# Kernel optimization log

Hardware: AMD Instinct MI355X
Metric: run time of the kernel (lower is better)

Reference implementation:

```python
import jax, jax.numpy as jnp
import numpy as np

BS, T_SEG, C, D, N, K, H = 4, 16, 64, 64, 4096, 32, 64
STRIDE = 4
NB, BSZ, NG, BPG = 4, 8, 1, 4  # K = NB*BSZ, NB = NG*BPG (dendritic tree covers all K)
EPS = 1e-8


def _forward(cc_signals, h_prev, prev_messages, trace_prim, trace_key,
             primitives, key_p, decay_logit, dendrite_branch_w, dendrite_group_w,
             fc1_w, fc1_b, fc2_w, fc2_b, mod_lr_logit, conn_indices):
    bs, n, d = h_prev.shape
    # ---- per-neuron modulator MLP: [h, trace_prim, trace_key, primitives, key] -> 3 ----
    mod_input = jnp.concatenate([
        h_prev, trace_prim, trace_key,
        jnp.broadcast_to(primitives[None], (bs, n, d)),
        jnp.broadcast_to(key_p[None], (bs, n, d))], axis=-1)           # [BS,N,5D]
    x = jnp.tanh(jnp.einsum('bnd,ndh->bnh', mod_input, fc1_w) + fc1_b)  # [BS,N,H]
    out3 = jnp.einsum('bnh,nho->bno', x, fc2_w) + fc2_b                 # [BS,N,3]
    gate_prim = jnp.tanh(out3[..., 0:1])
    gate_key = jnp.tanh(out3[..., 1:2])
    decay_mod = out3[..., 2]

    mod_lr = jax.nn.sigmoid(mod_lr_logit)
    tp_dir = trace_prim / jnp.clip(jnp.linalg.norm(trace_prim, axis=-1, keepdims=True), EPS)
    tk_dir = trace_key / jnp.clip(jnp.linalg.norm(trace_key, axis=-1, keepdims=True), EPS)
    eff_prim = primitives[None] + mod_lr * gate_prim * tp_dir           # [BS,N,D]
    eff_key = key_p[None] + mod_lr * gate_key * tk_dir                  # [BS,N,D]
    eff_decay = jax.nn.sigmoid(decay_logit[None] + decay_mod)[..., None]  # [BS,N,1]

    # routing computed once per segment from the initial messages
    routing = jax.nn.sigmoid(
        jnp.einsum('bnd,bnkd->bnk', eff_key, prev_messages[:, conn_indices]))  # [BS,N,K]

    def gather_fc(weighted):  # [BS,N,K,D] -> [BS,N,D] hierarchical dendritic reduce
        tree = weighted.reshape(bs, n, NB, BSZ, d)
        branch = jnp.tanh(jnp.einsum('bnjkd,njkd->bnjd', tree, dendrite_branch_w))  # [BS,N,NB,D]
        grouped = branch.reshape(bs, n, NG, BPG, d)
        group = jnp.tanh(jnp.einsum('bngpd,ngpd->bngd', grouped, dendrite_group_w))  # [BS,N,NG,D]
        return group.mean(axis=2)  # n_tree == K so no leftover term

    cc_steps = jnp.moveaxis(cc_signals[:, ::STRIDE], 0, 1)  # [n_steps,BS,C,D]

    def step(carry, cc_t):
        h, prev_msg = carry
        nm = prev_msg[:, conn_indices]                      # neighbor gather [BS,N,K,D]
        received = gather_fc(routing[..., None] * nm)       # [BS,N,D]
        received = received.at[:, :C].add(cc_t)             # inject port signals
        h = eff_decay * h + (1.0 - eff_decay) * received
        prev_msg = jnp.tanh(h * eff_prim)
        return (h, prev_msg), prev_msg[:, :C]

    (h_final, _), ports = jax.lax.scan(step, (h_prev, prev_messages), cc_steps)
    # each port output is held for `stride` tokens; only the fresh one carries grad
    ports_rep = jnp.repeat(ports, STRIDE, axis=0)            # [T,BS,C,D]
    fresh = (jnp.arange(T_SEG) % STRIDE == 0)[:, None, None, None]
    out = jnp.where(fresh, ports_rep, jax.lax.stop_gradient(ports_rep))
    return jnp.moveaxis(out, 0, 1)                           # [BS,T_seg,C,D]


def setup_inputs() -> dict:
    key = jax.random.key(0)
    ks = jax.random.split(key, 10)

    def rms_init(k, shape):
        raw = jax.random.normal(k, shape, dtype=jnp.float32)
        rms = jnp.clip(jnp.sqrt(jnp.mean(raw ** 2, axis=-1, keepdims=True)), EPS)
        return raw / rms

    cc_signals = jax.random.normal(ks[0], (BS, T_SEG, C, D), dtype=jnp.float32)
    h_prev = 0.1 * jax.random.normal(ks[1], (BS, N, D), dtype=jnp.float32)
    primitives = rms_init(ks[2], (N, D))
    key_p = rms_init(ks[3], (N, D))
    prev_messages = jnp.tanh(h_prev * primitives[None])
    trace_prim = 0.1 * jax.random.normal(ks[4], (BS, N, D), dtype=jnp.float32)
    trace_key = 0.1 * jax.random.normal(ks[5], (BS, N, D), dtype=jnp.float32)
    decay_logit = jnp.zeros((N,), dtype=jnp.float32)
    dendrite_branch_w = jnp.full((N, NB, BSZ, D), 1.0 / BSZ, dtype=jnp.float32)
    dendrite_group_w = jnp.full((N, NG, BPG, D), 1.0 / BPG, dtype=jnp.float32)
    fc1_w = jax.random.normal(ks[6], (N, 5 * D, H), dtype=jnp.float32) * (2.0 / (5 * D + H)) ** 0.5
    fc1_b = jnp.zeros((N, H), dtype=jnp.float32)
    fc2_w = 0.02 * jax.random.normal(ks[7], (N, H, 3), dtype=jnp.float32)
    fc2_b = jnp.zeros((N, 3), dtype=jnp.float32)
    mod_lr_logit = jnp.float32(-2.0)
    conn_indices = jnp.sort(jax.random.randint(ks[8], (N, K), 0, N, dtype=jnp.int32), axis=-1)
    return dict(cc_signals=cc_signals, h_prev=h_prev, prev_messages=prev_messages,
                trace_prim=trace_prim, trace_key=trace_key, primitives=primitives,
                key_p=key_p, decay_logit=decay_logit,
                dendrite_branch_w=dendrite_branch_w, dendrite_group_w=dendrite_group_w,
                fc1_w=fc1_w, fc1_b=fc1_b, fc2_w=fc2_w, fc2_b=fc2_b,
                mod_lr_logit=mod_lr_logit, conn_indices=conn_indices)


def reference(cc_signals, h_prev, prev_messages, trace_prim, trace_key,
              primitives, key_p, decay_logit, dendrite_branch_w, dendrite_group_w,
              fc1_w, fc1_b, fc2_w, fc2_b, mod_lr_logit, conn_indices):
    return _forward(cc_signals, h_prev, prev_messages, trace_prim, trace_key,
                    primitives, key_p, decay_logit, dendrite_branch_w, dendrite_group_w,
                    fc1_w, fc1_b, fc2_w, fc2_b, mod_lr_logit, conn_indices)
```

## Files before the change

### kernel.cpp

```cpp
#include <hip/hip_runtime.h>
#include <math.h>

#define BS 4
#define TSEG 16
#define CC 64
#define DD 64
#define NN 4096
#define KK 32
#define HH 64
#define D5 320

__device__ __forceinline__ float sigm(float x){ return 1.0f/(1.0f+expf(-x)); }
__device__ __forceinline__ float4 tanh4(float4 v){
    return make_float4(tanhf(v.x), tanhf(v.y), tanhf(v.z), tanhf(v.w));
}

__global__ __launch_bounds__(256) void k_pre(
    const float* __restrict__ h_prev,
    const float* __restrict__ pm0,
    const float* __restrict__ trp,
    const float* __restrict__ trk,
    const float* __restrict__ prim,
    const float* __restrict__ keyp,
    const float* __restrict__ dlog,
    const float* __restrict__ fc1w,
    const float* __restrict__ fc1b,
    const float* __restrict__ fc2w,
    const float* __restrict__ fc2b,
    const float* __restrict__ mll,
    const int*  __restrict__ conn,
    float* __restrict__ ws_ep,
    float* __restrict__ ws_rt,
    float* __restrict__ ws_ed)
{
    __shared__ float mod2[4][D5][4];
    __shared__ float ek_s[4][4][DD];
    __shared__ int   cn_s[4][KK];
    const int wid  = threadIdx.x >> 6;
    const int lane = threadIdx.x & 63;
    const int n    = (blockIdx.x << 2) + wid;

    #pragma unroll
    for (int b = 0; b < BS; b++) {
        mod2[wid][lane      ][b] = h_prev[((size_t)b*NN + n)*DD + lane];
        mod2[wid][64  + lane][b] = trp  [((size_t)b*NN + n)*DD + lane];
        mod2[wid][128 + lane][b] = trk  [((size_t)b*NN + n)*DD + lane];
    }
    {
        const float pv = prim[(size_t)n*DD + lane];
        const float kv = keyp[(size_t)n*DD + lane];
        #pragma unroll
        for (int b = 0; b < BS; b++) {
            mod2[wid][192 + lane][b] = pv;
            mod2[wid][256 + lane][b] = kv;
        }
    }
    if (lane < KK) cn_s[wid][lane] = conn[(size_t)n*KK + lane];

    const int g  = lane >> 4;
    const int hq = lane & 15;
    float acc[16];
    #pragma unroll
    for (int i = 0; i < 16; i++) acc[i] = 0.f;
    const float* wp = fc1w + (size_t)n*D5*HH + (size_t)g*HH + 4*hq;
    const float* mp = &mod2[wid][g][0];
    #pragma unroll 4
    for (int it = 0; it < 80; it++) {
        const float4 w4 = *(const float4*)(wp + (size_t)it*256);
        const float4 m4 = *(const float4*)(mp + it*16);
        acc[ 0] = fmaf(m4.x, w4.x, acc[ 0]);
        acc[ 1] = fmaf(m4.x, w4.y, acc[ 1]);
        acc[ 2] = fmaf(m4.x, w4.z, acc[ 2]);
        acc[ 3] = fmaf(m4.x, w4.w, acc[ 3]);
        acc[ 4] = fmaf(m4.y, w4.x, acc[ 4]);
        acc[ 5] = fmaf(m4.y, w4.y, acc[ 5]);
        acc[ 6] = fmaf(m4.y, w4.z, acc[ 6]);
        acc[ 7] = fmaf(m4.y, w4.w, acc[ 7]);
        acc[ 8] = fmaf(m4.z, w4.x, acc[ 8]);
        acc[ 9] = fmaf(m4.z, w4.y, acc[ 9]);
        acc[10] = fmaf(m4.z, w4.z, acc[10]);
        acc[11] = fmaf(m4.z, w4.w, acc[11]);
        acc[12] = fmaf(m4.w, w4.x, acc[12]);
        acc[13] = fmaf(m4.w, w4.y, acc[13]);
        acc[14] = fmaf(m4.w, w4.z, acc[14]);
        acc[15] = fmaf(m4.w, w4.w, acc[15]);
    }
    #pragma unroll
    for (int i = 0; i < 16; i++) {
        acc[i] += __shfl_xor(acc[i], 16, 64);
        acc[i] += __shfl_xor(acc[i], 32, 64);
    }
    const float4 b1 = *(const float4*)(fc1b + (size_t)n*HH + 4*hq);
    float x[16];
    #pragma unroll
    for (int b = 0; b < BS; b++) {
        x[b*4+0] = tanhf(acc[b*4+0] + b1.x);
        x[b*4+1] = tanhf(acc[b*4+1] + b1.y);
        x[b*4+2] = tanhf(acc[b*4+2] + b1.z);
        x[b*4+3] = tanhf(acc[b*4+3] + b1.w);
    }

    float f2[12];
    {
        const float4* f2p = (const float4*)(fc2w + (size_t)n*HH*3 + 12*hq);
        const float4 fa = f2p[0], fb = f2p[1], fc = f2p[2];
        f2[0]=fa.x; f2[1]=fa.y; f2[2]=fa.z; f2[3]=fa.w;
        f2[4]=fb.x; f2[5]=fb.y; f2[6]=fb.z; f2[7]=fb.w;
        f2[8]=fc.x; f2[9]=fc.y; f2[10]=fc.z; f2[11]=fc.w;
    }
    float po[12];
    #pragma unroll
    for (int b = 0; b < BS; b++) {
        #pragma unroll
        for (int o = 0; o < 3; o++) {
            po[b*3+o] = x[b*4+0]*f2[0*3+o] + x[b*4+1]*f2[1*3+o]
                      + x[b*4+2]*f2[2*3+o] + x[b*4+3]*f2[3*3+o];
        }
    }
    #pragma unroll
    for (int m = 1; m < 16; m <<= 1) {
        #pragma unroll
        for (int i = 0; i < 12; i++) po[i] += __shfl_xor(po[i], m, 64);
    }
    const float c0 = fc2b[(size_t)n*3+0];
    const float c1 = fc2b[(size_t)n*3+1];
    const float c2 = fc2b[(size_t)n*3+2];
    const float dl  = dlog[n];
    const float mlr = sigm(mll[0]);
    float gp[4], gk[4], ed[4];
    #pragma unroll
    for (int b = 0; b < BS; b++) {
        gp[b] = tanhf(po[b*3+0] + c0);
        gk[b] = tanhf(po[b*3+1] + c1);
        ed[b] = sigm(dl + po[b*3+2] + c2);
    }
    if (lane < 4) {
        const float edsel = (lane==0)?ed[0]:(lane==1)?ed[1]:(lane==2)?ed[2]:ed[3];
        ws_ed[(size_t)lane*NN + n] = edsel;
    }

    {
        const int d = lane;
        const float4 tpv = *(const float4*)(&mod2[wid][64  + d][0]);
        const float4 tkv = *(const float4*)(&mod2[wid][128 + d][0]);
        const float  pr  = mod2[wid][192 + d][0];
        const float  kp  = mod2[wid][256 + d][0];
        float tp[4] = {tpv.x, tpv.y, tpv.z, tpv.w};
        float tk[4] = {tkv.x, tkv.y, tkv.z, tkv.w};
        float s2[8];
        #pragma unroll
        for (int b = 0; b < BS; b++) { s2[b] = tp[b]*tp[b]; s2[4+b] = tk[b]*tk[b]; }
        #pragma unroll
        for (int m = 1; m < 64; m <<= 1) {
            #pragma unroll
            for (int i = 0; i < 8; i++) s2[i] += __shfl_xor(s2[i], m, 64);
        }
        #pragma unroll
        for (int b = 0; b < BS; b++) {
            const float np = fmaxf(sqrtf(s2[b]),   1e-8f);
            const float nk = fmaxf(sqrtf(s2[4+b]), 1e-8f);
            const float ep = pr + mlr*gp[b]*(tp[b]/np);
            const float ek = kp + mlr*gk[b]*(tk[b]/nk);
            ws_ep[((size_t)b*NN + n)*DD + d] = ep;
            ek_s[wid][b][d] = ek;
        }
    }

    {
        const int bb = lane >> 4, dq = lane & 15;
        const float4 ekq = *(const float4*)(&ek_s[wid][bb][4*dq]);
        #pragma unroll 8
        for (int k = 0; k < KK; k++) {
            const int cn = cn_s[wid][k];
            const float4 pm4 = *(const float4*)(pm0 + ((size_t)bb*NN + cn)*DD + 4*dq);
            float rr = ekq.x*pm4.x + ekq.y*pm4.y + ekq.z*pm4.z + ekq.w*pm4.w;
            rr += __shfl_xor(rr, 1, 64);
            rr += __shfl_xor(rr, 2, 64);
            rr += __shfl_xor(rr, 4, 64);
            rr += __shfl_xor(rr, 8, 64);
            if (dq == 0) ws_rt[((size_t)bb*NN + n)*KK + k] = sigm(rr);
        }
    }
}

__global__ __launch_bounds__(256) void k_step(
    const float* __restrict__ pm_in,
    float* __restrict__ pm_out,
    const float* __restrict__ h_in,
    float* __restrict__ h_out,
    const float* __restrict__ ws_ep,
    const float* __restrict__ ws_rt,
    const float* __restrict__ ws_ed,
    const float* __restrict__ bw,
    const float* __restrict__ gw,
    const int*  __restrict__ conn,
    const float* __restrict__ cc,
    float* __restrict__ out,
    const int s)
{
    __shared__ float bw_s[4][2048];
    __shared__ float gw_s[4][256];
    __shared__ float rt_s[4][4][KK];
    __shared__ int   cn_s[4][KK];
    const int wid  = threadIdx.x >> 6;
    const int lane = threadIdx.x & 63;
    const int n    = (blockIdx.x << 2) + wid;

    {
        const float4* src = (const float4*)(bw + (size_t)n*2048);
        float4* dst = (float4*)bw_s[wid];
        #pragma unroll
        for (int i = 0; i < 8; i++) dst[i*64 + lane] = src[i*64 + lane];
        ((float4*)gw_s[wid])[lane] = ((const float4*)(gw + (size_t)n*256))[lane];
        rt_s[wid][lane>>5][lane&31] =
            ws_rt[((size_t)(lane>>5)*NN + n)*KK + (lane&31)];
        rt_s[wid][2+(lane>>5)][lane&31] =
            ws_rt[((size_t)(2+(lane>>5))*NN + n)*KK + (lane&31)];
        if (lane < KK) cn_s[wid][lane] = conn[(size_t)n*KK + lane];
    }

    const int b = lane >> 4, dq = lane & 15;
    const int d0 = 4*dq;
    const size_t bnd = ((size_t)b*NN + n)*DD + d0;

    float4 bs[4];
    #pragma unroll
    for (int j = 0; j < 4; j++) bs[j] = make_float4(0.f,0.f,0.f,0.f);
    #pragma unroll
    for (int k = 0; k < KK; k++) {
        const int cn = cn_s[wid][k];
        const float4 nm = *(const float4*)(pm_in + ((size_t)b*NN + cn)*DD + d0);
        const float  w  = rt_s[wid][b][k];
        const float4 bv = *(const float4*)(&bw_s[wid][k*DD + d0]);
        const int j = k >> 3;
        bs[j].x = fmaf(w*nm.x, bv.x, bs[j].x);
        bs[j].y = fmaf(w*nm.y, bv.y, bs[j].y);
        bs[j].z = fmaf(w*nm.z, bv.z, bs[j].z);
        bs[j].w = fmaf(w*nm.w, bv.w, bs[j].w);
    }
    float4 gs = make_float4(0.f,0.f,0.f,0.f);
    #pragma unroll
    for (int j = 0; j < 4; j++) {
        const float4 br = tanh4(bs[j]);
        const float4 gv = *(const float4*)(&gw_s[wid][j*DD + d0]);
        gs.x = fmaf(br.x, gv.x, gs.x);
        gs.y = fmaf(br.y, gv.y, gs.y);
        gs.z = fmaf(br.z, gv.z, gs.z);
        gs.w = fmaf(br.w, gv.w, gs.w);
    }
    float4 recv = tanh4(gs);
    if (n < CC) {
        const float4 cv = *(const float4*)(cc + (size_t)((b*TSEG + 4*s)*CC + n)*DD + d0);
        recv.x += cv.x; recv.y += cv.y; recv.z += cv.z; recv.w += cv.w;
    }
    const float edv = ws_ed[(size_t)b*NN + n];
    float4 h = *(const float4*)(h_in + bnd);
    h.x = edv*h.x + (1.f-edv)*recv.x;
    h.y = edv*h.y + (1.f-edv)*recv.y;
    h.z = edv*h.z + (1.f-edv)*recv.z;
    h.w = edv*h.w + (1.f-edv)*recv.w;
    *(float4*)(h_out + bnd) = h;
    const float4 ep = *(const float4*)(ws_ep + bnd);
    const float4 pm = tanh4(make_float4(h.x*ep.x, h.y*ep.y, h.z*ep.z, h.w*ep.w));
    *(float4*)(pm_out + bnd) = pm;
    if (n < CC) {
        #pragma unroll
        for (int r = 0; r < 4; r++)
            *(float4*)(out + (size_t)((b*TSEG + 4*s + r)*CC + n)*DD + d0) = pm;
    }
}

extern "C" void kernel_launch(void* const* d_in, const int* in_sizes, int n_in,
                              void* d_out, int out_size, void* d_ws, size_t ws_size,
                              hipStream_t stream) {
    const float* cc    = (const float*)d_in[0];
    const float* h_prev= (const float*)d_in[1];
    const float* pm0   = (const float*)d_in[2];
    const float* trp   = (const float*)d_in[3];
    const float* trk   = (const float*)d_in[4];
    const float* prim  = (const float*)d_in[5];
    const float* keyp  = (const float*)d_in[6];
    const float* dlog  = (const float*)d_in[7];
    const float* bw    = (const float*)d_in[8];
    const float* gw    = (const float*)d_in[9];
    const float* fc1w  = (const float*)d_in[10];
    const float* fc1b  = (const float*)d_in[11];
    const float* fc2w  = (const float*)d_in[12];
    const float* fc2b  = (const float*)d_in[13];
    const float* mll   = (const float*)d_in[14];
    const int*   conn  = (const int*)d_in[15];
    float* out = (float*)d_out;

    float* ws   = (float*)d_ws;
    const size_t BND = (size_t)BS*NN*DD;
    float* ws_h  = ws;
    float* ws_ep = ws + BND;
    float* msgA  = ws + 2*BND;
    float* msgB  = ws + 3*BND;
    float* ws_rt = ws + 4*BND;
    float* ws_ed = ws + 4*BND + (size_t)BS*NN*KK;

    k_pre<<<NN/4, 256, 0, stream>>>(h_prev, pm0, trp, trk, prim, keyp, dlog,
                                    fc1w, fc1b, fc2w, fc2b, mll, conn,
                                    ws_ep, ws_rt, ws_ed);

    k_step<<<NN/4, 256, 0, stream>>>(pm0,  msgA, h_prev, ws_h, ws_ep, ws_rt, ws_ed,
                                     bw, gw, conn, cc, out, 0);
    k_step<<<NN/4, 256, 0, stream>>>(msgA, msgB, ws_h, ws_h, ws_ep, ws_rt, ws_ed,
                                     bw, gw, conn, cc, out, 1);
    k_step<<<NN/4, 256, 0, stream>>>(msgB, msgA, ws_h, ws_h, ws_ep, ws_rt, ws_ed,
                                     bw, gw, conn, cc, out, 2);
    k_step<<<NN/4, 256, 0, stream>>>(msgA, msgB, ws_h, ws_h, ws_ep, ws_rt, ws_ed,
                                     bw, gw, conn, cc, out, 3);
}
```

Measured before the change: 618.1 us.

## Fuse pre-pass and four step kernels into one cooperative persistent kernel

Merges the modulator/routing pre-pass and the four recurrent step kernels into a single cooperative kernel that uses grid-wide syncs between steps. h, eff_prim, decay and routing stay in registers or LDS instead of round-tripping through workspace, and the dendrite weights are loaded into shared memory once rather than four times. The fc1 weight stream now uses nontemporal loads. The cost is grid.sync overhead and a residency requirement: 1024 blocks with about 38KB of LDS each must all be co-resident. If the cooperative launch fails, the code falls back to the old multi-kernel path.

Result: slower. 1.577 ms (+155.2%).

```diff
diff --git a/kernel.cpp b/kernel.cpp
--- a/kernel.cpp
+++ b/kernel.cpp
@@ -1,5 +1,8 @@
 #include <hip/hip_runtime.h>
+#include <hip/hip_cooperative_groups.h>
 #include <math.h>
+
+namespace cg = cooperative_groups;
 
 #define BS 4
 #define TSEG 16
@@ -10,12 +13,19 @@
 #define HH 64
 #define D5 320
 
+typedef float nat_f4 __attribute__((ext_vector_type(4)));
+
 __device__ __forceinline__ float sigm(float x){ return 1.0f/(1.0f+expf(-x)); }
 __device__ __forceinline__ float4 tanh4(float4 v){
     return make_float4(tanhf(v.x), tanhf(v.y), tanhf(v.z), tanhf(v.w));
 }
-
-__global__ __launch_bounds__(256) void k_pre(
+__device__ __forceinline__ float4 ntload4(const float* p){
+    nat_f4 v = __builtin_nontemporal_load((const nat_f4*)p);
+    return make_float4(v.x, v.y, v.z, v.w);
+}
+
+__global__ __launch_bounds__(256, 4) void k_fused(
+    const float* __restrict__ cc,
     const float* __restrict__ h_prev,
     const float* __restrict__ pm0,
     const float* __restrict__ trp,
@@ -23,36 +33,45 @@
     const float* __restrict__ prim,
     const float* __restrict__ keyp,
     const float* __restrict__ dlog,
+    const float* __restrict__ bw,
+    const float* __restrict__ gw,
     const float* __restrict__ fc1w,
     const float* __restrict__ fc1b,
     const float* __restrict__ fc2w,
     const float* __restrict__ fc2b,
     const float* __restrict__ mll,
     const int*  __restrict__ conn,
-    float* __restrict__ ws_ep,
-    float* __restrict__ ws_rt,
-    float* __restrict__ ws_ed)
+    float* __restrict__ msgA,
+    float* __restrict__ msgB,
+    float* __restrict__ out)
 {
-    __shared__ float mod2[4][D5][4];
-    __shared__ float ek_s[4][4][DD];
+    __shared__ __align__(16) char smem[36864];
+    __shared__ float rt_s[4][4][KK];
     __shared__ int   cn_s[4][KK];
+    float* mod2 = (float*)smem;
+    float* ep_s = (float*)(smem + 20480);
+    float* bw_s = (float*)smem;
+    float* gw_s = (float*)(smem + 32768);
+
     const int wid  = threadIdx.x >> 6;
     const int lane = threadIdx.x & 63;
     const int n    = (blockIdx.x << 2) + wid;
 
-    #pragma unroll
-    for (int b = 0; b < BS; b++) {
-        mod2[wid][lane      ][b] = h_prev[((size_t)b*NN + n)*DD + lane];
-        mod2[wid][64  + lane][b] = trp  [((size_t)b*NN + n)*DD + lane];
-        mod2[wid][128 + lane][b] = trk  [((size_t)b*NN + n)*DD + lane];
+#define MOD2(d,b) mod2[(((wid)*320 + (d))<<2) + (b)]
+
+    #pragma unroll
+    for (int b = 0; b < BS; b++) {
+        MOD2(lane,       b) = h_prev[((size_t)b*NN + n)*DD + lane];
+        MOD2(64  + lane, b) = trp  [((size_t)b*NN + n)*DD + lane];
+        MOD2(128 + lane, b) = trk  [((size_t)b*NN + n)*DD + lane];
     }
     {
         const float pv = prim[(size_t)n*DD + lane];
         const float kv = keyp[(size_t)n*DD + lane];
         #pragma unroll
         for (int b = 0; b < BS; b++) {
-            mod2[wid][192 + lane][b] = pv;
-            mod2[wid][256 + lane][b] = kv;
+            MOD2(192 + lane, b) = pv;
+            MOD2(256 + lane, b) = kv;
         }
     }
     if (lane < KK) cn_s[wid][lane] = conn[(size_t)n*KK + lane];
@@ -63,10 +82,10 @@
     #pragma unroll
     for (int i = 0; i < 16; i++) acc[i] = 0.f;
     const float* wp = fc1w + (size_t)n*D5*HH + (size_t)g*HH + 4*hq;
-    const float* mp = &mod2[wid][g][0];
+    const float* mp = &MOD2(g, 0);
     #pragma unroll 4
     for (int it = 0; it < 80; it++) {
-        const float4 w4 = *(const float4*)(wp + (size_t)it*256);
+        const float4 w4 = ntload4(wp + (size_t)it*256);
         const float4 m4 = *(const float4*)(mp + it*16);
         acc[ 0] = fmaf(m4.x, w4.x, acc[ 0]);
         acc[ 1] = fmaf(m4.x, w4.y, acc[ 1]);
@@ -134,17 +153,14 @@
         gk[b] = tanhf(po[b*3+1] + c1);
         ed[b] = sigm(dl + po[b*3+2] + c2);
     }
-    if (lane < 4) {
-        const float edsel = (lane==0)?ed[0]:(lane==1)?ed[1]:(lane==2)?ed[2]:ed[3];
-        ws_ed[(size_t)lane*NN + n] = edsel;
-    }
-
+
+    float ekreg[4];
     {
         const int d = lane;
-        const float4 tpv = *(const float4*)(&mod2[wid][64  + d][0]);
-        const float4 tkv = *(const float4*)(&mod2[wid][128 + d][0]);
-        const float  pr  = mod2[wid][192 + d][0];
-        const float  kp  = mod2[wid][256 + d][0];
+        const float4 tpv = *(const float4*)(&MOD2(64  + d, 0));
+        const float4 tkv = *(const float4*)(&MOD2(128 + d, 0));
+        const float  pr  = MOD2(192 + d, 0);
+        const float  kp  = MOD2(256 + d, 0);
         float tp[4] = {tpv.x, tpv.y, tpv.z, tpv.w};
         float tk[4] = {tkv.x, tkv.y, tkv.z, tkv.w};
         float s2[8];
@@ -159,13 +175,216 @@
         for (int b = 0; b < BS; b++) {
             const float np = fmaxf(sqrtf(s2[b]),   1e-8f);
             const float nk = fmaxf(sqrtf(s2[4+b]), 1e-8f);
-            const float ep = pr + mlr*gp[b]*(tp[b]/np);
-            const float ek = kp + mlr*gk[b]*(tk[b]/nk);
-            ws_ep[((size_t)b*NN + n)*DD + d] = ep;
-            ek_s[wid][b][d] = ek;
-        }
-    }
-
+            ep_s[((wid*4 + b)<<6) + d] = pr + mlr*gp[b]*(tp[b]/np);
+            ekreg[b] = kp + mlr*gk[b]*(tk[b]/nk);
+        }
+    }
+
+    {
+        const int d = lane;
+        #pragma unroll
+        for (int b = 0; b < BS; b++) MOD2(64 + d, b) = ekreg[b];
+    }
+    {
+        const int bb = lane >> 4, dq = lane & 15;
+        float ekq[4];
+        #pragma unroll
+        for (int i = 0; i < 4; i++) ekq[i] = MOD2(64 + 4*dq + i, bb);
+        #pragma unroll 8
+        for (int k = 0; k < KK; k++) {
+            const int cn = cn_s[wid][k];
+            const float4 pm4 = *(const float4*)(pm0 + ((size_t)bb*NN + cn)*DD + 4*dq);
+            float rr = ekq[0]*pm4.x + ekq[1]*pm4.y + ekq[2]*pm4.z + ekq[3]*pm4.w;
+            rr += __shfl_xor(rr, 1, 64);
+            rr += __shfl_xor(rr, 2, 64);
+            rr += __shfl_xor(rr, 4, 64);
+            rr += __shfl_xor(rr, 8, 64);
+            if (dq == 0) rt_s[wid][bb][k] = sigm(rr);
+        }
+    }
+
+    const int b  = lane >> 4;
+    const int d0 = 4*(lane & 15);
+    const float edv = (b==0)?ed[0]:(b==1)?ed[1]:(b==2)?ed[2]:ed[3];
+    float4 h, ep4;
+    h.x = MOD2(d0+0, b); h.y = MOD2(d0+1, b);
+    h.z = MOD2(d0+2, b); h.w = MOD2(d0+3, b);
+    ep4 = *(const float4*)(&ep_s[((wid*4 + b)<<6) + d0]);
+
+    __syncthreads();
+
+    {
+        const float4* src = (const float4*)(bw + (size_t)n*2048);
+        float4* dst = (float4*)(bw_s + wid*2048);
+        #pragma unroll
+        for (int i = 0; i < 8; i++) dst[i*64 + lane] = src[i*64 + lane];
+        ((float4*)(gw_s + wid*256))[lane] = ((const float4*)(gw + (size_t)n*256))[lane];
+    }
+
+    cg::grid_group grid = cg::this_grid();
+    const size_t bnd = ((size_t)b*NN + n)*DD + d0;
+    const float* pin = pm0;
+    #pragma unroll
+    for (int s = 0; s < 4; s++) {
+        float4 bsa[4];
+        #pragma unroll
+        for (int j = 0; j < 4; j++) bsa[j] = make_float4(0.f,0.f,0.f,0.f);
+        #pragma unroll
+        for (int k = 0; k < KK; k++) {
+            const int cn = cn_s[wid][k];
+            const float4 nm = *(const float4*)(pin + ((size_t)b*NN + cn)*DD + d0);
+            const float  w  = rt_s[wid][b][k];
+            const float4 bv = *(const float4*)(&bw_s[wid*2048 + k*DD + d0]);
+            const int j = k >> 3;
+            bsa[j].x = fmaf(w*nm.x, bv.x, bsa[j].x);
+            bsa[j].y = fmaf(w*nm.y, bv.y, bsa[j].y);
+            bsa[j].z = fmaf(w*nm.z, bv.z, bsa[j].z);
+            bsa[j].w = fmaf(w*nm.w, bv.w, bsa[j].w);
+        }
+        float4 gs = make_float4(0.f,0.f,0.f,0.f);
+        #pragma unroll
+        for (int j = 0; j < 4; j++) {
+            const float4 br = tanh4(bsa[j]);
+            const float4 gv = *(const float4*)(&gw_s[wid*256 + j*DD + d0]);
+            gs.x = fmaf(br.x, gv.x, gs.x);
+            gs.y = fmaf(br.y, gv.y, gs.y);
+            gs.z = fmaf(br.z, gv.z, gs.z);
+            gs.w = fmaf(br.w, gv.w, gs.w);
+        }
+        float4 recv = tanh4(gs);
+        if (n < CC) {
+            const float4 cv = *(const float4*)(cc + (size_t)((b*TSEG + 4*s)*CC + n)*DD + d0);
+            recv.x += cv.x; recv.y += cv.y; recv.z += cv.z; recv.w += cv.w;
+        }
+        h.x = edv*h.x + (1.f-edv)*recv.x;
+        h.y = edv*h.y + (1.f-edv)*recv.y;
+        h.z = edv*h.z + (1.f-edv)*recv.z;
+        h.w = edv*h.w + (1.f-edv)*recv.w;
+        const float4 pm = tanh4(make_float4(h.x*ep4.x, h.y*ep4.y, h.z*ep4.z, h.w*ep4.w));
+        if (s < 3) {
+            float* pout = (s & 1) ? msgB : msgA;
+            *(float4*)(pout + bnd) = pm;
+        }
+        if (n < CC) {
+            #pragma unroll
+            for (int r = 0; r < 4; r++)
+                *(float4*)(out + (size_t)((b*TSEG + 4*s + r)*CC + n)*DD + d0) = pm;
+        }
+        if (s < 3) {
+            __threadfence();
+            grid.sync();
+            pin = (s & 1) ? msgB : msgA;
+        }
+    }
+#undef MOD2
+}
+
+__global__ __launch_bounds__(256) void k_pre(
+    const float* __restrict__ h_prev, const float* __restrict__ pm0,
+    const float* __restrict__ trp, const float* __restrict__ trk,
+    const float* __restrict__ prim, const float* __restrict__ keyp,
+    const float* __restrict__ dlog, const float* __restrict__ fc1w,
+    const float* __restrict__ fc1b, const float* __restrict__ fc2w,
+    const float* __restrict__ fc2b, const float* __restrict__ mll,
+    const int*  __restrict__ conn, float* __restrict__ ws_ep,
+    float* __restrict__ ws_rt, float* __restrict__ ws_ed)
+{
+    __shared__ float mod2[4][D5][4];
+    __shared__ float ek_s[4][4][DD];
+    __shared__ int   cn_s[4][KK];
+    const int wid  = threadIdx.x >> 6;
+    const int lane = threadIdx.x & 63;
+    const int n    = (blockIdx.x << 2) + wid;
+    #pragma unroll
+    for (int b = 0; b < BS; b++) {
+        mod2[wid][lane      ][b] = h_prev[((size_t)b*NN + n)*DD + lane];
+        mod2[wid][64  + lane][b] = trp  [((size_t)b*NN + n)*DD + lane];
+        mod2[wid][128 + lane][b] = trk  [((size_t)b*NN + n)*DD + lane];
+    }
+    {
+        const float pv = prim[(size_t)n*DD + lane];
+        const float kv = keyp[(size_t)n*DD + lane];
+        #pragma unroll
+        for (int b = 0; b < BS; b++) { mod2[wid][192+lane][b]=pv; mod2[wid][256+lane][b]=kv; }
+    }
+    if (lane < KK) cn_s[wid][lane] = conn[(size_t)n*KK + lane];
+    const int g = lane >> 4, hq = lane & 15;
+    float acc[16];
+    #pragma unroll
+    for (int i = 0; i < 16; i++) acc[i] = 0.f;
+    const float* wp = fc1w + (size_t)n*D5*HH + (size_t)g*HH + 4*hq;
+    const float* mp = &mod2[wid][g][0];
+    #pragma unroll 4
+    for (int it = 0; it < 80; it++) {
+        const float4 w4 = *(const float4*)(wp + (size_t)it*256);
+        const float4 m4 = *(const float4*)(mp + it*16);
+        acc[0]=fmaf(m4.x,w4.x,acc[0]);   acc[1]=fmaf(m4.x,w4.y,acc[1]);
+        acc[2]=fmaf(m4.x,w4.z,acc[2]);   acc[3]=fmaf(m4.x,w4.w,acc[3]);
+        acc[4]=fmaf(m4.y,w4.x,acc[4]);   acc[5]=fmaf(m4.y,w4.y,acc[5]);
+        acc[6]=fmaf(m4.y,w4.z,acc[6]);   acc[7]=fmaf(m4.y,w4.w,acc[7]);
+        acc[8]=fmaf(m4.z,w4.x,acc[8]);   acc[9]=fmaf(m4.z,w4.y,acc[9]);
+        acc[10]=fmaf(m4.z,w4.z,acc[10]); acc[11]=fmaf(m4.z,w4.w,acc[11]);
+        acc[12]=fmaf(m4.w,w4.x,acc[12]); acc[13]=fmaf(m4.w,w4.y,acc[13]);
+        acc[14]=fmaf(m4.w,w4.z,acc[14]); acc[15]=fmaf(m4.w,w4.w,acc[15]);
+    }
+    #pragma unroll
+    for (int i = 0; i < 16; i++) { acc[i]+=__shfl_xor(acc[i],16,64); acc[i]+=__shfl_xor(acc[i],32,64); }
+    const float4 b1 = *(const float4*)(fc1b + (size_t)n*HH + 4*hq);
+    float x[16];
+    #pragma unroll
+    for (int b = 0; b < BS; b++) {
+        x[b*4+0]=tanhf(acc[b*4+0]+b1.x); x[b*4+1]=tanhf(acc[b*4+1]+b1.y);
+        x[b*4+2]=tanhf(acc[b*4+2]+b1.z); x[b*4+3]=tanhf(acc[b*4+3]+b1.w);
+    }
+    float f2[12];
+    {
+        const float4* f2p = (const float4*)(fc2w + (size_t)n*HH*3 + 12*hq);
+        const float4 fa=f2p[0], fb=f2p[1], fc=f2p[2];
+        f2[0]=fa.x; f2[1]=fa.y; f2[2]=fa.z; f2[3]=fa.w;
+        f2[4]=fb.x; f2[5]=fb.y; f2[6]=fb.z; f2[7]=fb.w;
+        f2[8]=fc.x; f2[9]=fc.y; f2[10]=fc.z; f2[11]=fc.w;
+    }
+    float po[12];
+    #pragma unroll
+    for (int b = 0; b < BS; b++)
+        #pragma unroll
+        for (int o = 0; o < 3; o++)
+            po[b*3+o] = x[b*4+0]*f2[o] + x[b*4+1]*f2[3+o] + x[b*4+2]*f2[6+o] + x[b*4+3]*f2[9+o];
+    #pragma unroll
+    for (int m = 1; m < 16; m <<= 1)
+        #pragma unroll
+        for (int i = 0; i < 12; i++) po[i] += __shfl_xor(po[i], m, 64);
+    const float c0=fc2b[(size_t)n*3+0], c1=fc2b[(size_t)n*3+1], c2=fc2b[(size_t)n*3+2];
+    const float dl=dlog[n], mlr=sigm(mll[0]);
+    float gp[4], gk[4], ed[4];
+    #pragma unroll
+    for (int b = 0; b < BS; b++) {
+        gp[b]=tanhf(po[b*3+0]+c0); gk[b]=tanhf(po[b*3+1]+c1); ed[b]=sigm(dl+po[b*3+2]+c2);
+    }
+    if (lane < 4) {
+        const float e=(lane==0)?ed[0]:(lane==1)?ed[1]:(lane==2)?ed[2]:ed[3];
+        ws_ed[(size_t)lane*NN + n] = e;
+    }
+    {
+        const int d = lane;
+        const float4 tpv=*(const float4*)(&mod2[wid][64+d][0]);
+        const float4 tkv=*(const float4*)(&mod2[wid][128+d][0]);
+        const float pr=mod2[wid][192+d][0], kp=mod2[wid][256+d][0];
+        float tp[4]={tpv.x,tpv.y,tpv.z,tpv.w}, tk[4]={tkv.x,tkv.y,tkv.z,tkv.w};
+        float s2[8];
+        #pragma unroll
+        for (int b = 0; b < BS; b++) { s2[b]=tp[b]*tp[b]; s2[4+b]=tk[b]*tk[b]; }
+        #pragma unroll
+        for (int m = 1; m < 64; m <<= 1)
+            #pragma unroll
+            for (int i = 0; i < 8; i++) s2[i] += __shfl_xor(s2[i], m, 64);
+        #pragma unroll
+        for (int b = 0; b < BS; b++) {
+            const float np=fmaxf(sqrtf(s2[b]),1e-8f), nk=fmaxf(sqrtf(s2[4+b]),1e-8f);
+            ws_ep[((size_t)b*NN+n)*DD+d] = pr + mlr*gp[b]*(tp[b]/np);
+            ek_s[wid][b][d] = kp + mlr*gk[b]*(tk[b]/nk);
+        }
+    }
     {
         const int bb = lane >> 4, dq = lane & 15;
         const float4 ekq = *(const float4*)(&ek_s[wid][bb][4*dq]);
@@ -174,91 +393,69 @@
             const int cn = cn_s[wid][k];
             const float4 pm4 = *(const float4*)(pm0 + ((size_t)bb*NN + cn)*DD + 4*dq);
             float rr = ekq.x*pm4.x + ekq.y*pm4.y + ekq.z*pm4.z + ekq.w*pm4.w;
-            rr += __shfl_xor(rr, 1, 64);
-            rr += __shfl_xor(rr, 2, 64);
-            rr += __shfl_xor(rr, 4, 64);
-            rr += __shfl_xor(rr, 8, 64);
+            rr+=__shfl_xor(rr,1,64); rr+=__shfl_xor(rr,2,64);
+            rr+=__shfl_xor(rr,4,64); rr+=__shfl_xor(rr,8,64);
             if (dq == 0) ws_rt[((size_t)bb*NN + n)*KK + k] = sigm(rr);
         }
     }
 }
 
 __global__ __launch_bounds__(256) void k_step(
-    const float* __restrict__ pm_in,
-    float* __restrict__ pm_out,
-    const float* __restrict__ h_in,
-    float* __restrict__ h_out,
-    const float* __restrict__ ws_ep,
-    const float* __restrict__ ws_rt,
-    const float* __restrict__ ws_ed,
-    const float* __restrict__ bw,
-    const float* __restrict__ gw,
-    const int*  __restrict__ conn,
-    const float* __restrict__ cc,
-    float* __restrict__ out,
-    const int s)
+    const float* __restrict__ pm_in, float* __restrict__ pm_out,
+    const float* __restrict__ h_in, float* __restrict__ h_out,
+    const float* __restrict__ ws_ep, const float* __restrict__ ws_rt,
+    const float* __restrict__ ws_ed, const float* __restrict__ bw,
+    const float* __restrict__ gw, const int* __restrict__ conn,
+    const float* __restrict__ cc, float* __restrict__ out, const int s)
 {
     __shared__ float bw_s[4][2048];
     __shared__ float gw_s[4][256];
     __shared__ float rt_s[4][4][KK];
     __shared__ int   cn_s[4][KK];
-    const int wid  = threadIdx.x >> 6;
-    const int lane = threadIdx.x & 63;
-    const int n    = (blockIdx.x << 2) + wid;
-
+    const int wid = threadIdx.x >> 6, lane = threadIdx.x & 63;
+    const int n = (blockIdx.x << 2) + wid;
     {
         const float4* src = (const float4*)(bw + (size_t)n*2048);
         float4* dst = (float4*)bw_s[wid];
         #pragma unroll
         for (int i = 0; i < 8; i++) dst[i*64 + lane] = src[i*64 + lane];
         ((float4*)gw_s[wid])[lane] = ((const float4*)(gw + (size_t)n*256))[lane];
-        rt_s[wid][lane>>5][lane&31] =
-            ws_rt[((size_t)(lane>>5)*NN + n)*KK + (lane&31)];
-        rt_s[wid][2+(lane>>5)][lane&31] =
-            ws_rt[((size_t)(2+(lane>>5))*NN + n)*KK + (lane&31)];
+        rt_s[wid][lane>>5][lane&31] = ws_rt[((size_t)(lane>>5)*NN + n)*KK + (lane&31)];
+        rt_s[wid][2+(lane>>5)][lane&31] = ws_rt[((size_t)(2+(lane>>5))*NN + n)*KK + (lane&31)];
         if (lane < KK) cn_s[wid][lane] = conn[(size_t)n*KK + lane];
     }
-
-    const int b = lane >> 4, dq = lane & 15;
-    const int d0 = 4*dq;
+    const int b = lane >> 4, dq = lane & 15, d0 = 4*dq;
     const size_t bnd = ((size_t)b*NN + n)*DD + d0;
-
-    float4 bs[4];
-    #pragma unroll
-    for (int j = 0; j < 4; j++) bs[j] = make_float4(0.f,0.f,0.f,0.f);
+    float4 bsa[4];
+    #pragma unroll
+    for (int j = 0; j < 4; j++) bsa[j] = make_float4(0.f,0.f,0.f,0.f);
     #pragma unroll
     for (int k = 0; k < KK; k++) {
         const int cn = cn_s[wid][k];
         const float4 nm = *(const float4*)(pm_in + ((size_t)b*NN + cn)*DD + d0);
-        const float  w  = rt_s[wid][b][k];
+        const float w = rt_s[wid][b][k];
         const float4 bv = *(const float4*)(&bw_s[wid][k*DD + d0]);
         const int j = k >> 3;
-        bs[j].x = fmaf(w*nm.x, bv.x, bs[j].x);
-        bs[j].y = fmaf(w*nm.y, bv.y, bs[j].y);
-        bs[j].z = fmaf(w*nm.z, bv.z, bs[j].z);
-        bs[j].w = fmaf(w*nm.w, bv.w, bs[j].w);
+        bsa[j].x=fmaf(w*nm.x,bv.x,bsa[j].x); bsa[j].y=fmaf(w*nm.y,bv.y,bsa[j].y);
+        bsa[j].z=fmaf(w*nm.z,bv.z,bsa[j].z); bsa[j].w=fmaf(w*nm.w,bv.w,bsa[j].w);
     }
     float4 gs = make_float4(0.f,0.f,0.f,0.f);
     #pragma unroll
     for (int j = 0; j < 4; j++) {
-        const float4 br = tanh4(bs[j]);
+        const float4 br = tanh4(bsa[j]);
         const float4 gv = *(const float4*)(&gw_s[wid][j*DD + d0]);
-        gs.x = fmaf(br.x, gv.x, gs.x);
-        gs.y = fmaf(br.y, gv.y, gs.y);
-        gs.z = fmaf(br.z, gv.z, gs.z);
-        gs.w = fmaf(br.w, gv.w, gs.w);
+        gs.x=fmaf(br.x,gv.x,gs.x); gs.y=fmaf(br.y,gv.y,gs.y);
+        gs.z=fmaf(br.z,gv.z,gs.z); gs.w=fmaf(br.w,gv.w,gs.w);
     }
     float4 recv = tanh4(gs);
     if (n < CC) {
         const float4 cv = *(const float4*)(cc + (size_t)((b*TSEG + 4*s)*CC + n)*DD + d0);
-        recv.x += cv.x; recv.y += cv.y; recv.z += cv.z; recv.w += cv.w;
+        recv.x+=cv.x; recv.y+=cv.y; recv.z+=cv.z; recv.w+=cv.w;
     }
     const float edv = ws_ed[(size_t)b*NN + n];
     float4 h = *(const float4*)(h_in + bnd);
-    h.x = edv*h.x + (1.f-edv)*recv.x;
-    h.y = edv*h.y + (1.f-edv)*recv.y;
-    h.z = edv*h.z + (1.f-edv)*recv.z;
-    h.w = edv*h.w + (1.f-edv)*recv.w;
+    h.x=edv*h.x+(1.f-edv)*recv.x; h.y=edv*h.y+(1.f-edv)*recv.y;
+    h.z=edv*h.z+(1.f-edv)*recv.z; h.w=edv*h.w+(1.f-edv)*recv.w;
     *(float4*)(h_out + bnd) = h;
     const float4 ep = *(const float4*)(ws_ep + bnd);
     const float4 pm = tanh4(make_float4(h.x*ep.x, h.y*ep.y, h.z*ep.z, h.w*ep.w));
@@ -291,25 +488,35 @@
     const int*   conn  = (const int*)d_in[15];
     float* out = (float*)d_out;
 
-    float* ws   = (float*)d_ws;
+    float* ws = (float*)d_ws;
     const size_t BND = (size_t)BS*NN*DD;
-    float* ws_h  = ws;
-    float* ws_ep = ws + BND;
-    float* msgA  = ws + 2*BND;
-    float* msgB  = ws + 3*BND;
+    float* msgA  = ws;
+    float* msgB  = ws + BND;
+    float* ws_h  = ws + 2*BND;
+    float* ws_ep = ws + 3*BND;
     float* ws_rt = ws + 4*BND;
     float* ws_ed = ws + 4*BND + (size_t)BS*NN*KK;
 
-    k_pre<<<NN/4, 256, 0, stream>>>(h_prev, pm0, trp, trk, prim, keyp, dlog,
-                                    fc1w, fc1b, fc2w, fc2b, mll, conn,
-                                    ws_ep, ws_rt, ws_ed);
-
-    k_step<<<NN/4, 256, 0, stream>>>(pm0,  msgA, h_prev, ws_h, ws_ep, ws_rt, ws_ed,
-                                     bw, gw, conn, cc, out, 0);
-    k_step<<<NN/4, 256, 0, stream>>>(msgA, msgB, ws_h, ws_h, ws_ep, ws_rt, ws_ed,
-                                     bw, gw, conn, cc, out, 1);
-    k_step<<<NN/4, 256, 0, stream>>>(msgB, msgA, ws_h, ws_h, ws_ep, ws_rt, ws_ed,
-                                     bw, gw, conn, cc, out, 2);
-    k_step<<<NN/4, 256, 0, stream>>>(msgA, msgB, ws_h, ws_h, ws_ep, ws_rt, ws_ed,
-                                     bw, gw, conn, cc, out, 3);
+    void* args[] = { (void*)&cc, (void*)&h_prev, (void*)&pm0, (void*)&trp,
+                     (void*)&trk, (void*)&prim, (void*)&keyp, (void*)&dlog,
+                     (void*)&bw, (void*)&gw, (void*)&fc1w, (void*)&fc1b,
+                     (void*)&fc2w, (void*)&fc2b, (void*)&mll, (void*)&conn,
+                     (void*)&msgA, (void*)&msgB, (void*)&out };
+    hipError_t err = hipLaunchCooperativeKernel((void*)k_fused,
+                                                dim3(NN/4), dim3(256),
+                                                args, 0, stream);
+    if (err != hipSuccess) {
+        (void)hipGetLastError();
+        k_pre<<<NN/4, 256, 0, stream>>>(h_prev, pm0, trp, trk, prim, keyp, dlog,
+                                        fc1w, fc1b, fc2w, fc2b, mll, conn,
+                                        ws_ep, ws_rt, ws_ed);
+        k_step<<<NN/4, 256, 0, stream>>>(pm0,  msgA, h_prev, ws_h, ws_ep, ws_rt, ws_ed,
+                                         bw, gw, conn, cc, out, 0);
+        k_step<<<NN/4, 256, 0, stream>>>(msgA, msgB, ws_h, ws_h, ws_ep, ws_rt, ws_ed,
+                                         bw, gw, conn, cc, out, 1);
+        k_step<<<NN/4, 256, 0, stream>>>(msgB, msgA, ws_h, ws_h, ws_ep, ws_rt, ws_ed,
+                                         bw, gw, conn, cc, out, 2);
+        k_step<<<NN/4, 256, 0, stream>>>(msgA, msgB, ws_h, ws_h, ws_ep, ws_rt, ws_ed,
+                                         bw, gw, conn, cc, out, 3);
+    }
 }
```

## Fuse first recurrent step into precompute kernel, drop LDS weight staging

Applied to the files above, without the earlier changes.

The precompute kernel now also runs step 0, reusing h, ep and routing values already held in shared memory and registers. This removes one launch and the global round trip for those intermediates. The step kernel reads dendrite weights straight from global memory instead of staging them in LDS, which lowers LDS use per block and may allow more blocks to be resident. The fc1 weight stream uses nontemporal loads to avoid polluting the cache. The fused kernel uses more registers and shared memory, which could lower its occupancy.

New measurement: 652.0 us. 5.5% more time.

```diff
diff --git a/kernel.cpp b/kernel.cpp
--- a/kernel.cpp
+++ b/kernel.cpp
@@ -10,12 +10,19 @@
 #define HH 64
 #define D5 320
 
+typedef float nat_f4 __attribute__((ext_vector_type(4)));
+
 __device__ __forceinline__ float sigm(float x){ return 1.0f/(1.0f+expf(-x)); }
 __device__ __forceinline__ float4 tanh4(float4 v){
     return make_float4(tanhf(v.x), tanhf(v.y), tanhf(v.z), tanhf(v.w));
 }
-
-__global__ __launch_bounds__(256) void k_pre(
+__device__ __forceinline__ float4 ntload4(const float* p){
+    nat_f4 v = __builtin_nontemporal_load((const nat_f4*)p);
+    return make_float4(v.x, v.y, v.z, v.w);
+}
+
+__global__ __launch_bounds__(256) void k_pre_step0(
+    const float* __restrict__ cc,
     const float* __restrict__ h_prev,
     const float* __restrict__ pm0,
     const float* __restrict__ trp,
@@ -23,18 +30,25 @@
     const float* __restrict__ prim,
     const float* __restrict__ keyp,
     const float* __restrict__ dlog,
+    const float* __restrict__ bw,
+    const float* __restrict__ gw,
     const float* __restrict__ fc1w,
     const float* __restrict__ fc1b,
     const float* __restrict__ fc2w,
     const float* __restrict__ fc2b,
     const float* __restrict__ mll,
     const int*  __restrict__ conn,
+    float* __restrict__ ws_h,
     float* __restrict__ ws_ep,
     float* __restrict__ ws_rt,
-    float* __restrict__ ws_ed)
+    float* __restrict__ ws_ed,
+    float* __restrict__ msgA,
+    float* __restrict__ out)
 {
     __shared__ float mod2[4][D5][4];
     __shared__ float ek_s[4][4][DD];
+    __shared__ float ep_s[4][4][DD];
+    __shared__ float rt_s[4][4][KK];
     __shared__ int   cn_s[4][KK];
     const int wid  = threadIdx.x >> 6;
     const int lane = threadIdx.x & 63;
@@ -66,24 +80,16 @@
     const float* mp = &mod2[wid][g][0];
     #pragma unroll 4
     for (int it = 0; it < 80; it++) {
-        const float4 w4 = *(const float4*)(wp + (size_t)it*256);
+        const float4 w4 = ntload4(wp + (size_t)it*256);
         const float4 m4 = *(const float4*)(mp + it*16);
-        acc[ 0] = fmaf(m4.x, w4.x, acc[ 0]);
-        acc[ 1] = fmaf(m4.x, w4.y, acc[ 1]);
-        acc[ 2] = fmaf(m4.x, w4.z, acc[ 2]);
-        acc[ 3] = fmaf(m4.x, w4.w, acc[ 3]);
-        acc[ 4] = fmaf(m4.y, w4.x, acc[ 4]);
-        acc[ 5] = fmaf(m4.y, w4.y, acc[ 5]);
-        acc[ 6] = fmaf(m4.y, w4.z, acc[ 6]);
-        acc[ 7] = fmaf(m4.y, w4.w, acc[ 7]);
-        acc[ 8] = fmaf(m4.z, w4.x, acc[ 8]);
-        acc[ 9] = fmaf(m4.z, w4.y, acc[ 9]);
-        acc[10] = fmaf(m4.z, w4.z, acc[10]);
-        acc[11] = fmaf(m4.z, w4.w, acc[11]);
-        acc[12] = fmaf(m4.w, w4.x, acc[12]);
-        acc[13] = fmaf(m4.w, w4.y, acc[13]);
-        acc[14] = fmaf(m4.w, w4.z, acc[14]);
-        acc[15] = fmaf(m4.w, w4.w, acc[15]);
+        acc[0]=fmaf(m4.x,w4.x,acc[0]);   acc[1]=fmaf(m4.x,w4.y,acc[1]);
+        acc[2]=fmaf(m4.x,w4.z,acc[2]);   acc[3]=fmaf(m4.x,w4.w,acc[3]);
+        acc[4]=fmaf(m4.y,w4.x,acc[4]);   acc[5]=fmaf(m4.y,w4.y,acc[5]);
+        acc[6]=fmaf(m4.y,w4.z,acc[6]);   acc[7]=fmaf(m4.y,w4.w,acc[7]);
+        acc[8]=fmaf(m4.z,w4.x,acc[8]);   acc[9]=fmaf(m4.z,w4.y,acc[9]);
+        acc[10]=fmaf(m4.z,w4.z,acc[10]); acc[11]=fmaf(m4.z,w4.w,acc[11]);
+        acc[12]=fmaf(m4.w,w4.x,acc[12]); acc[13]=fmaf(m4.w,w4.y,acc[13]);
+        acc[14]=fmaf(m4.w,w4.z,acc[14]); acc[15]=fmaf(m4.w,w4.w,acc[15]);
     }
     #pragma unroll
     for (int i = 0; i < 16; i++) {
@@ -112,10 +118,9 @@
     #pragma unroll
     for (int b = 0; b < BS; b++) {
         #pragma unroll
-        for (int o = 0; o < 3; o++) {
-            po[b*3+o] = x[b*4+0]*f2[0*3+o] + x[b*4+1]*f2[1*3+o]
-                      + x[b*4+2]*f2[2*3+o] + x[b*4+3]*f2[3*3+o];
-        }
+        for (int o = 0; o < 3; o++)
+            po[b*3+o] = x[b*4+0]*f2[o] + x[b*4+1]*f2[3+o]
+                      + x[b*4+2]*f2[6+o] + x[b*4+3]*f2[9+o];
     }
     #pragma unroll
     for (int m = 1; m < 16; m <<= 1) {
@@ -135,8 +140,8 @@
         ed[b] = sigm(dl + po[b*3+2] + c2);
     }
     if (lane < 4) {
-        const float edsel = (lane==0)?ed[0]:(lane==1)?ed[1]:(lane==2)?ed[2]:ed[3];
-        ws_ed[(size_t)lane*NN + n] = edsel;
+        const float e = (lane==0)?ed[0]:(lane==1)?ed[1]:(lane==2)?ed[2]:ed[3];
+        ws_ed[(size_t)lane*NN + n] = e;
     }
 
     {
@@ -160,34 +165,89 @@
             const float np = fmaxf(sqrtf(s2[b]),   1e-8f);
             const float nk = fmaxf(sqrtf(s2[4+b]), 1e-8f);
             const float ep = pr + mlr*gp[b]*(tp[b]/np);
-            const float ek = kp + mlr*gk[b]*(tk[b]/nk);
+            ep_s[wid][b][d] = ep;
             ws_ep[((size_t)b*NN + n)*DD + d] = ep;
-            ek_s[wid][b][d] = ek;
+            ek_s[wid][b][d] = kp + mlr*gk[b]*(tk[b]/nk);
         }
     }
 
-    {
-        const int bb = lane >> 4, dq = lane & 15;
-        const float4 ekq = *(const float4*)(&ek_s[wid][bb][4*dq]);
+    const int b  = lane >> 4;
+    const int dq = lane & 15;
+    const int d0 = 4*dq;
+    {
+        const float4 ekq = *(const float4*)(&ek_s[wid][b][d0]);
         #pragma unroll 8
         for (int k = 0; k < KK; k++) {
             const int cn = cn_s[wid][k];
-            const float4 pm4 = *(const float4*)(pm0 + ((size_t)bb*NN + cn)*DD + 4*dq);
+            const float4 pm4 = *(const float4*)(pm0 + ((size_t)b*NN + cn)*DD + d0);
             float rr = ekq.x*pm4.x + ekq.y*pm4.y + ekq.z*pm4.z + ekq.w*pm4.w;
             rr += __shfl_xor(rr, 1, 64);
             rr += __shfl_xor(rr, 2, 64);
             rr += __shfl_xor(rr, 4, 64);
             rr += __shfl_xor(rr, 8, 64);
-            if (dq == 0) ws_rt[((size_t)bb*NN + n)*KK + k] = sigm(rr);
+            if (dq == 0) {
+                const float rv = sigm(rr);
+                rt_s[wid][b][k] = rv;
+                ws_rt[((size_t)b*NN + n)*KK + k] = rv;
+            }
         }
+    }
+
+    const size_t bnd = ((size_t)b*NN + n)*DD + d0;
+    const float edv = (b==0)?ed[0]:(b==1)?ed[1]:(b==2)?ed[2]:ed[3];
+    float4 h;
+    h.x = mod2[wid][d0+0][b]; h.y = mod2[wid][d0+1][b];
+    h.z = mod2[wid][d0+2][b]; h.w = mod2[wid][d0+3][b];
+    const float4 ep4 = *(const float4*)(&ep_s[wid][b][d0]);
+
+    float4 bsa[4];
+    #pragma unroll
+    for (int j = 0; j < 4; j++) bsa[j] = make_float4(0.f,0.f,0.f,0.f);
+    #pragma unroll
+    for (int k = 0; k < KK; k++) {
+        const int cn = cn_s[wid][k];
+        const float4 nm = *(const float4*)(pm0 + ((size_t)b*NN + cn)*DD + d0);
+        const float  w  = rt_s[wid][b][k];
+        const float4 bv = *(const float4*)(bw + (size_t)n*2048 + k*DD + d0);
+        const int j = k >> 3;
+        bsa[j].x = fmaf(w*nm.x, bv.x, bsa[j].x);
+        bsa[j].y = fmaf(w*nm.y, bv.y, bsa[j].y);
+        bsa[j].z = fmaf(w*nm.z, bv.z, bsa[j].z);
+        bsa[j].w = fmaf(w*nm.w, bv.w, bsa[j].w);
+    }
+    float4 gs = make_float4(0.f,0.f,0.f,0.f);
+    #pragma unroll
+    for (int j = 0; j < 4; j++) {
+        const float4 br = tanh4(bsa[j]);
+        const float4 gv = *(const float4*)(gw + (size_t)n*256 + j*DD + d0);
+        gs.x = fmaf(br.x, gv.x, gs.x);
+        gs.y = fmaf(br.y, gv.y, gs.y);
+        gs.z = fmaf(br.z, gv.z, gs.z);
+        gs.w = fmaf(br.w, gv.w, gs.w);
+    }
+    float4 recv = tanh4(gs);
+    if (n < CC) {
+        const float4 cv = *(const float4*)(cc + (size_t)((b*TSEG)*CC + n)*DD + d0);
+        recv.x += cv.x; recv.y += cv.y; recv.z += cv.z; recv.w += cv.w;
+    }
+    h.x = edv*h.x + (1.f-edv)*recv.x;
+    h.y = edv*h.y + (1.f-edv)*recv.y;
+    h.z = edv*h.z + (1.f-edv)*recv.z;
+    h.w = edv*h.w + (1.f-edv)*recv.w;
+    *(float4*)(ws_h + bnd) = h;
+    const float4 pm = tanh4(make_float4(h.x*ep4.x, h.y*ep4.y, h.z*ep4.z, h.w*ep4.w));
+    *(float4*)(msgA + bnd) = pm;
+    if (n < CC) {
+        #pragma unroll
+        for (int r = 0; r < 4; r++)
+            *(float4*)(out + (size_t)((b*TSEG + r)*CC + n)*DD + d0) = pm;
     }
 }
 
 __global__ __launch_bounds__(256) void k_step(
     const float* __restrict__ pm_in,
     float* __restrict__ pm_out,
-    const float* __restrict__ h_in,
-    float* __restrict__ h_out,
+    float* __restrict__ ws_h,
     const float* __restrict__ ws_ep,
     const float* __restrict__ ws_rt,
     const float* __restrict__ ws_ed,
@@ -198,51 +258,41 @@
     float* __restrict__ out,
     const int s)
 {
-    __shared__ float bw_s[4][2048];
-    __shared__ float gw_s[4][256];
     __shared__ float rt_s[4][4][KK];
     __shared__ int   cn_s[4][KK];
     const int wid  = threadIdx.x >> 6;
     const int lane = threadIdx.x & 63;
     const int n    = (blockIdx.x << 2) + wid;
-
-    {
-        const float4* src = (const float4*)(bw + (size_t)n*2048);
-        float4* dst = (float4*)bw_s[wid];
-        #pragma unroll
-        for (int i = 0; i < 8; i++) dst[i*64 + lane] = src[i*64 + lane];
-        ((float4*)gw_s[wid])[lane] = ((const float4*)(gw + (size_t)n*256))[lane];
+    {
         rt_s[wid][lane>>5][lane&31] =
             ws_rt[((size_t)(lane>>5)*NN + n)*KK + (lane&31)];
         rt_s[wid][2+(lane>>5)][lane&31] =
             ws_rt[((size_t)(2+(lane>>5))*NN + n)*KK + (lane&31)];
         if (lane < KK) cn_s[wid][lane] = conn[(size_t)n*KK + lane];
     }
-
-    const int b = lane >> 4, dq = lane & 15;
-    const int d0 = 4*dq;
+    const int b = lane >> 4, dq = lane & 15, d0 = 4*dq;
     const size_t bnd = ((size_t)b*NN + n)*DD + d0;
 
-    float4 bs[4];
-    #pragma unroll
-    for (int j = 0; j < 4; j++) bs[j] = make_float4(0.f,0.f,0.f,0.f);
+    float4 bsa[4];
+    #pragma unroll
+    for (int j = 0; j < 4; j++) bsa[j] = make_float4(0.f,0.f,0.f,0.f);
     #pragma unroll
     for (int k = 0; k < KK; k++) {
         const int cn = cn_s[wid][k];
         const float4 nm = *(const float4*)(pm_in + ((size_t)b*NN + cn)*DD + d0);
         const float  w  = rt_s[wid][b][k];
-        const float4 bv = *(const float4*)(&bw_s[wid][k*DD + d0]);
+        const float4 bv = *(const float4*)(bw + (size_t)n*2048 + k*DD + d0);
         const int j = k >> 3;
-        bs[j].x = fmaf(w*nm.x, bv.x, bs[j].x);
-        bs[j].y = fmaf(w*nm.y, bv.y, bs[j].y);
-        bs[j].z = fmaf(w*nm.z, bv.z, bs[j].z);
-        bs[j].w = fmaf(w*nm.w, bv.w, bs[j].w);
+        bsa[j].x = fmaf(w*nm.x, bv.x, bsa[j].x);
+        bsa[j].y = fmaf(w*nm.y, bv.y, bsa[j].y);
+        bsa[j].z = fmaf(w*nm.z, bv.z, bsa[j].z);
+        bsa[j].w = fmaf(w*nm.w, bv.w, bsa[j].w);
     }
     float4 gs = make_float4(0.f,0.f,0.f,0.f);
     #pragma unroll
     for (int j = 0; j < 4; j++) {
-        const float4 br = tanh4(bs[j]);
-        const float4 gv = *(const float4*)(&gw_s[wid][j*DD + d0]);
+        const float4 br = tanh4(bsa[j]);
+        const float4 gv = *(const float4*)(gw + (size_t)n*256 + j*DD + d0);
         gs.x = fmaf(br.x, gv.x, gs.x);
         gs.y = fmaf(br.y, gv.y, gs.y);
         gs.z = fmaf(br.z, gv.z, gs.z);
@@ -254,12 +304,12 @@
         recv.x += cv.x; recv.y += cv.y; recv.z += cv.z; recv.w += cv.w;
     }
     const float edv = ws_ed[(size_t)b*NN + n];
-    float4 h = *(const float4*)(h_in + bnd);
+    float4 h = *(const float4*)(ws_h + bnd);
     h.x = edv*h.x + (1.f-edv)*recv.x;
     h.y = edv*h.y + (1.f-edv)*recv.y;
     h.z = edv*h.z + (1.f-edv)*recv.z;
     h.w = edv*h.w + (1.f-edv)*recv.w;
-    *(float4*)(h_out + bnd) = h;
+    *(float4*)(ws_h + bnd) = h;
     const float4 ep = *(const float4*)(ws_ep + bnd);
     const float4 pm = tanh4(make_float4(h.x*ep.x, h.y*ep.y, h.z*ep.z, h.w*ep.w));
     *(float4*)(pm_out + bnd) = pm;
@@ -291,25 +341,23 @@
     const int*   conn  = (const int*)d_in[15];
     float* out = (float*)d_out;
 
-    float* ws   = (float*)d_ws;
+    float* ws = (float*)d_ws;
     const size_t BND = (size_t)BS*NN*DD;
-    float* ws_h  = ws;
-    float* ws_ep = ws + BND;
-    float* msgA  = ws + 2*BND;
-    float* msgB  = ws + 3*BND;
+    float* msgA  = ws;
+    float* msgB  = ws + BND;
+    float* ws_h  = ws + 2*BND;
+    float* ws_ep = ws + 3*BND;
     float* ws_rt = ws + 4*BND;
     float* ws_ed = ws + 4*BND + (size_t)BS*NN*KK;
 
-    k_pre<<<NN/4, 256, 0, stream>>>(h_prev, pm0, trp, trk, prim, keyp, dlog,
-                                    fc1w, fc1b, fc2w, fc2b, mll, conn,
-                                    ws_ep, ws_rt, ws_ed);
-
-    k_step<<<NN/4, 256, 0, stream>>>(pm0,  msgA, h_prev, ws_h, ws_ep, ws_rt, ws_ed,
-                                     bw, gw, conn, cc, out, 0);
-    k_step<<<NN/4, 256, 0, stream>>>(msgA, msgB, ws_h, ws_h, ws_ep, ws_rt, ws_ed,
+    k_pre_step0<<<NN/4, 256, 0, stream>>>(cc, h_prev, pm0, trp, trk, prim, keyp,
+                                          dlog, bw, gw, fc1w, fc1b, fc2w, fc2b,
+                                          mll, conn, ws_h, ws_ep, ws_rt, ws_ed,
+                                          msgA, out);
+    k_step<<<NN/4, 256, 0, stream>>>(msgA, msgB, ws_h, ws_ep, ws_rt, ws_ed,
                                      bw, gw, conn, cc, out, 1);
-    k_step<<<NN/4, 256, 0, stream>>>(msgB, msgA, ws_h, ws_h, ws_ep, ws_rt, ws_ed,
+    k_step<<<NN/4, 256, 0, stream>>>(msgB, msgA, ws_h, ws_ep, ws_rt, ws_ed,
                                      bw, gw, conn, cc, out, 2);
-    k_step<<<NN/4, 256, 0, stream>>>(msgA, msgB, ws_h, ws_h, ws_ep, ws_rt, ws_ed,
+    k_step<<<NN/4, 256, 0, stream>>>(msgA, msgB, ws_h, ws_ep, ws_rt, ws_ed,
                                      bw, gw, conn, cc, out, 3);
 }
```
